# Performance work log

Hardware: AMD Instinct MI355X
Metric: run time of the kernel (lower is better)

Reference implementation:

```python
import jax, jax.numpy as jnp
import numpy as np

N = 262144  # collocation points
H = 128     # hidden width


def setup_inputs() -> dict:
    key = jax.random.key(0)
    ks = jax.random.split(key, 9)
    def glorot(k, shape):
        fan_in = shape[0]
        return jax.random.normal(k, shape, dtype=jnp.float32) / jnp.sqrt(jnp.float32(fan_in))
    return {
        "x": jax.random.normal(ks[0], (N, 3), dtype=jnp.float32),
        "W1": glorot(ks[1], (3, H)), "b1": jnp.zeros((H,), jnp.float32),
        "W2": glorot(ks[2], (H, H)), "b2": jnp.zeros((H,), jnp.float32),
        "W3": glorot(ks[3], (H, H)), "b3": jnp.zeros((H,), jnp.float32),
        "W4": glorot(ks[4], (H, 1)), "b4": jnp.zeros((1,), jnp.float32),
    }


def reference(x, W1, b1, W2, b2, W3, b3, W4, b4):
    def f(xi):  # xi: (3,) -> scalar c
        h = jnp.tanh(xi @ W1 + b1)
        h = jnp.tanh(h @ W2 + b2)
        h = jnp.tanh(h @ W3 + b3)
        return (h @ W4 + b4)[0]

    # forward value and full first-order gradient per point
    c, g = jax.vmap(jax.value_and_grad(f))(x)  # c: (N,), g: (N, 3)
    dc_dt, dc_dx, dc_dy = g[:, 0], g[:, 1], g[:, 2]

    # diagonal Hessian entries via forward-over-reverse HVPs
    e_x = jnp.array([0.0, 1.0, 0.0], dtype=x.dtype)
    e_y = jnp.array([0.0, 0.0, 1.0], dtype=x.dtype)

    def hvp(xi, v):
        return jax.jvp(jax.grad(f), (xi,), (v,))[1]

    d2c_dx2 = jax.vmap(lambda xi: hvp(xi, e_x)[1])(x)  # (N,)
    d2c_dy2 = jax.vmap(lambda xi: hvp(xi, e_y)[2])(x)  # (N,)

    return (c[:, None], dc_dt, dc_dx, dc_dy, d2c_dx2, d2c_dy2)
```

## Files before the change

### kernel.cpp

```cpp
#include <hip/hip_runtime.h>
#include <hip/hip_bf16.h>

#define TPB  256
#define WPB  4
#define NBLK 256
#define PROW 136
#define PSZ  (128 * PROW)

typedef short    short8 __attribute__((ext_vector_type(8)));
typedef float    f32x4  __attribute__((ext_vector_type(4)));
typedef unsigned uint4v __attribute__((ext_vector_type(4)));

#define SBAR() __builtin_amdgcn_sched_barrier(0)

struct Frag   { short8 k0, k1, k2, k3; };
struct Acc8   { f32x4 n0, n1, n2, n3, n4, n5, n6, n7; };
struct Acc8x6 { Acc8 a, b, c, d, e, f; };

__device__ __forceinline__ f32x4 sp4(float v) { f32x4 r = {v, v, v, v}; return r; }

__device__ __forceinline__ float fast_tanh(float z) {
    float e = __expf(2.0f * z);
    return 1.0f - 2.0f * __builtin_amdgcn_rcpf(e + 1.0f);
}
__device__ __forceinline__ f32x4 tanh4(f32x4 z) {
    f32x4 r;
    r[0] = fast_tanh(z[0]); r[1] = fast_tanh(z[1]);
    r[2] = fast_tanh(z[2]); r[3] = fast_tanh(z[3]);
    return r;
}

__device__ __forceinline__ unsigned short bf16_bits(float v) {
    __hip_bfloat16 b = __float2bfloat16(v);
    unsigned short s; __builtin_memcpy(&s, &b, 2);
    return s;
}
__device__ __forceinline__ unsigned pack_bf2(float lo, float hi) {
    return (unsigned)bf16_bits(lo) | ((unsigned)bf16_bits(hi) << 16);
}
__device__ __forceinline__ short8 packB(f32x4 lo, f32x4 hi) {
    uint4v u;
    u[0] = pack_bf2(lo[0], lo[1]);
    u[1] = pack_bf2(lo[2], lo[3]);
    u[2] = pack_bf2(hi[0], hi[1]);
    u[3] = pack_bf2(hi[2], hi[3]);
    return __builtin_bit_cast(short8, u);
}

__device__ __forceinline__ Acc8 acc_zero() {
    Acc8 A;
    A.n0 = sp4(0.f); A.n1 = sp4(0.f); A.n2 = sp4(0.f); A.n3 = sp4(0.f);
    A.n4 = sp4(0.f); A.n5 = sp4(0.f); A.n6 = sp4(0.f); A.n7 = sp4(0.f);
    return A;
}
__device__ __forceinline__ Acc8 acc_bias(const float* bp, int fb) {
    Acc8 A;
    A.n0 = *(const f32x4*)(bp + 0 * 16 + fb);
    A.n1 = *(const f32x4*)(bp + 1 * 16 + fb);
    A.n2 = *(const f32x4*)(bp + 2 * 16 + fb);
    A.n3 = *(const f32x4*)(bp + 3 * 16 + fb);
    A.n4 = *(const f32x4*)(bp + 4 * 16 + fb);
    A.n5 = *(const f32x4*)(bp + 5 * 16 + fb);
    A.n6 = *(const f32x4*)(bp + 6 * 16 + fb);
    A.n7 = *(const f32x4*)(bp + 7 * 16 + fb);
    return A;
}

__device__ __forceinline__ Acc8x6 gemm6_frag(const unsigned short* __restrict__ pnl,
                                             int c, int g,
                                             Frag B0, Frag B1, Frag B2,
                                             Frag B3, Frag B4, Frag B5,
                                             Acc8 A0, Acc8 A1, Acc8 A2,
                                             Acc8 A3, Acc8 A4, Acc8 A5) {
#define ROW6(NT, N, KK, V0, V1, V2, V3, V4, V5) { \
    const short8 af = *reinterpret_cast<const short8*>( \
        pnl + ((NT) * 16 + c) * PROW + (KK) * 32 + g * 8); \
    A0.N = __builtin_amdgcn_mfma_f32_16x16x32_bf16(af, V0, A0.N, 0, 0, 0); \
    A1.N = __builtin_amdgcn_mfma_f32_16x16x32_bf16(af, V1, A1.N, 0, 0, 0); \
    A2.N = __builtin_amdgcn_mfma_f32_16x16x32_bf16(af, V2, A2.N, 0, 0, 0); \
    A3.N = __builtin_amdgcn_mfma_f32_16x16x32_bf16(af, V3, A3.N, 0, 0, 0); \
    A4.N = __builtin_amdgcn_mfma_f32_16x16x32_bf16(af, V4, A4.N, 0, 0, 0); \
    A5.N = __builtin_amdgcn_mfma_f32_16x16x32_bf16(af, V5, A5.N, 0, 0, 0); }
#define KS6(KK, V0, V1, V2, V3, V4, V5) \
    ROW6(0, n0, KK, V0, V1, V2, V3, V4, V5) ROW6(1, n1, KK, V0, V1, V2, V3, V4, V5) \
    ROW6(2, n2, KK, V0, V1, V2, V3, V4, V5) ROW6(3, n3, KK, V0, V1, V2, V3, V4, V5) \
    ROW6(4, n4, KK, V0, V1, V2, V3, V4, V5) ROW6(5, n5, KK, V0, V1, V2, V3, V4, V5) \
    ROW6(6, n6, KK, V0, V1, V2, V3, V4, V5) ROW6(7, n7, KK, V0, V1, V2, V3, V4, V5) SBAR();
    KS6(0, B0.k0, B1.k0, B2.k0, B3.k0, B4.k0, B5.k0)
    KS6(1, B0.k1, B1.k1, B2.k1, B3.k1, B4.k1, B5.k1)
    KS6(2, B0.k2, B1.k2, B2.k2, B3.k2, B4.k2, B5.k2)
    KS6(3, B0.k3, B1.k3, B2.k3, B3.k3, B4.k3, B5.k3)
#undef KS6
#undef ROW6
    Acc8x6 R; R.a = A0; R.b = A1; R.c = A2; R.d = A3; R.e = A4; R.f = A5; return R;
}

__device__ __forceinline__ float red16(float v) {
    v += __shfl_xor(v, 16, 64);
    v += __shfl_xor(v, 32, 64);
    return v;
}
__device__ __forceinline__ float hsum4(f32x4 v) {
    return (v[0] + v[1]) + (v[2] + v[3]);
}

__global__ __launch_bounds__(TPB, 1) __attribute__((amdgpu_waves_per_eu(1)))
void mlp_jet_kernel(
    const float* __restrict__ X,
    const float* __restrict__ gW1, const float* __restrict__ gB1,
    const float* __restrict__ gW2, const float* __restrict__ gB2,
    const float* __restrict__ gW3, const float* __restrict__ gB3,
    const float* __restrict__ gW4, const float* __restrict__ gB4,
    float* __restrict__ out, int N)
{
    __shared__ alignas(16) unsigned short sPanel[2 * PSZ];
    __shared__ alignas(16) float sParam[7 * 128];

    const int tid = threadIdx.x;
    for (int idx = tid; idx < 2 * 128 * 128; idx += TPB) {
        int p = idx >> 14, e = idx & 16383, n = e >> 7, pp = e & 127;
        int kk = pp >> 5, gg = (pp >> 3) & 3, jj = pp & 7;
        int f = ((((jj >> 2) << 2) | kk) << 4) | (gg << 2) | (jj & 3);
        const float* Wsrc = p ? gW3 : gW2;
        sPanel[p * PSZ + n * PROW + pp] = bf16_bits(Wsrc[f * 128 + n]);
    }
    if (tid < 128) {
        sParam[0 * 128 + tid] = gW1[tid];
        sParam[1 * 128 + tid] = gW1[128 + tid];
        sParam[2 * 128 + tid] = gW1[256 + tid];
        sParam[3 * 128 + tid] = gB1[tid];
        sParam[4 * 128 + tid] = gB2[tid];
        sParam[5 * 128 + tid] = gB3[tid];
        sParam[6 * 128 + tid] = gW4[tid];
    }
    __syncthreads();

    const int lane = tid & 63;
    const int wave = tid >> 6;
    const int c = lane & 15, g = lane >> 4;
    const int fb = g << 2;
    const unsigned short* const pW2f = sPanel;
    const unsigned short* const pW3f = sPanel + PSZ;
    const float b4 = gB4[0];
    const float* const w4p = sParam + 6 * 128;

    const int tiles = N >> 4;
    for (int t = blockIdx.x * WPB + wave; t < tiles; t += NBLK * WPB) {
        const int sbase = t << 4;
        const float* xp = X + (long)(sbase + c) * 3;
        const float xt = xp[0], xx = xp[1], xy = xp[2];

        Frag h1F, t1t, t1x, t1y, s1x, s1y;
#define SEED(K, IL, IH) { \
    const int fL = (IL) * 16 + fb, fH = (IH) * 16 + fb; \
    f32x4 wtL = *(const f32x4*)(sParam + fL),        wtH = *(const f32x4*)(sParam + fH); \
    f32x4 wxL = *(const f32x4*)(sParam + 128 + fL),  wxH = *(const f32x4*)(sParam + 128 + fH); \
    f32x4 wyL = *(const f32x4*)(sParam + 256 + fL),  wyH = *(const f32x4*)(sParam + 256 + fH); \
    f32x4 bbL = *(const f32x4*)(sParam + 384 + fL),  bbH = *(const f32x4*)(sParam + 384 + fH); \
    f32x4 hL = tanh4(sp4(xt) * wtL + sp4(xx) * wxL + sp4(xy) * wyL + bbL); \
    f32x4 hH = tanh4(sp4(xt) * wtH + sp4(xx) * wxH + sp4(xy) * wyH + bbH); \
    f32x4 aL = sp4(1.f) - hL * hL, aH = sp4(1.f) - hH * hH; \
    h1F.K = packB(hL, hH); \
    t1t.K = packB(aL * wtL, aH * wtH); \
    t1x.K = packB(aL * wxL, aH * wxH); \
    t1y.K = packB(aL * wyL, aH * wyH); \
    s1x.K = packB((sp4(0.f) - hL) * aL * wxL * wxL, (sp4(0.f) - hH) * aH * wxH * wxH); \
    s1y.K = packB((sp4(0.f) - hL) * aL * wyL * wyL, (sp4(0.f) - hH) * aH * wyH * wyH); \
    SBAR(); }
        SEED(k0, 0, 4) SEED(k1, 1, 5) SEED(k2, 2, 6) SEED(k3, 3, 7)
#undef SEED

        Acc8x6 R6 = gemm6_frag(pW2f, c, g, h1F, t1t, t1x, t1y, s1x, s1y,
                               acc_bias(sParam + 4 * 128, fb),
                               acc_zero(), acc_zero(), acc_zero(),
                               acc_zero(), acc_zero());

        Frag h2F, t2t, txF, tyF, s2xF, s2yF;
#define POST2(K, NL, NH) { \
    f32x4 hL = tanh4(R6.a.NL), hH = tanh4(R6.a.NH); \
    f32x4 aL = sp4(1.f) - hL * hL, aH = sp4(1.f) - hH * hH; \
    h2F.K = packB(hL, hH); \
    t2t.K = packB(aL * R6.b.NL, aH * R6.b.NH); \
    f32x4 txL = aL * R6.c.NL, txH = aH * R6.c.NH; \
    txF.K = packB(txL, txH); \
    f32x4 pxL = (sp4(0.f) - hL) * txL * R6.c.NL, pxH = (sp4(0.f) - hH) * txH * R6.c.NH; \
    f32x4 tyL = aL * R6.d.NL, tyH = aH * R6.d.NH; \
    tyF.K = packB(tyL, tyH); \
    f32x4 pyL = (sp4(0.f) - hL) * tyL * R6.d.NL, pyH = (sp4(0.f) - hH) * tyH * R6.d.NH; \
    s2xF.K = packB(aL * R6.e.NL + pxL, aH * R6.e.NH + pxH); \
    s2yF.K = packB(aL * R6.f.NL + pyL, aH * R6.f.NH + pyH); \
    SBAR(); }
        POST2(k0, n0, n4) POST2(k1, n1, n5) POST2(k2, n2, n6) POST2(k3, n3, n7)
#undef POST2

        R6 = gemm6_frag(pW3f, c, g, h2F, t2t, txF, tyF, s2xF, s2yF,
                        acc_bias(sParam + 5 * 128, fb),
                        acc_zero(), acc_zero(), acc_zero(),
                        acc_zero(), acc_zero());

        {
            f32x4 scp = sp4(0.f), sc1t = sp4(0.f);
            f32x4 srxa = sp4(0.f), srxb = sp4(0.f);
            f32x4 srya = sp4(0.f), sryb = sp4(0.f);
            f32x4 sc2x = sp4(0.f), sc2y = sp4(0.f);
#define DOTS(NL, NH, IL, IH) { \
    f32x4 w4L = *(const f32x4*)(w4p + (IL) * 16 + fb); \
    f32x4 w4H = *(const f32x4*)(w4p + (IH) * 16 + fb); \
    f32x4 hL = tanh4(R6.a.NL), hH = tanh4(R6.a.NH); \
    f32x4 waL = w4L * (sp4(1.f) - hL * hL), waH = w4H * (sp4(1.f) - hH * hH); \
    scp  += w4L * hL + w4H * hH; \
    sc1t += waL * R6.b.NL + waH * R6.b.NH; \
    srxa += waL * R6.c.NL + waH * R6.c.NH; \
    srxb -= waL * hL * R6.c.NL * R6.c.NL + waH * hH * R6.c.NH * R6.c.NH; \
    srya += waL * R6.d.NL + waH * R6.d.NH; \
    sryb -= waL * hL * R6.d.NL * R6.d.NL + waH * hH * R6.d.NH * R6.d.NH; \
    sc2x += waL * R6.e.NL + waH * R6.e.NH; \
    sc2y += waL * R6.f.NL + waH * R6.f.NH; \
    SBAR(); }
            DOTS(n0, n4, 0, 4) DOTS(n1, n5, 1, 5) DOTS(n2, n6, 2, 6) DOTS(n3, n7, 3, 7)
#undef DOTS
            float cp  = red16(hsum4(scp));
            float c1t = red16(hsum4(sc1t));
            float c1x = red16(hsum4(srxa));
            float c1y = red16(hsum4(srya));
            float c2x = red16(hsum4(srxb) + hsum4(sc2x));
            float c2y = red16(hsum4(sryb) + hsum4(sc2y));
            if (lane < 16) {
                out[sbase + lane]           = cp + b4;
                out[(long)N + sbase + lane] = c1t;
                out[2L * N + sbase + lane]  = c1x;
                out[3L * N + sbase + lane]  = c1y;
                out[4L * N + sbase + lane]  = 2.f * c2x;
                out[5L * N + sbase + lane]  = 2.f * c2y;
            }
        }
    }
}

extern "C" void kernel_launch(void* const* d_in, const int* in_sizes, int n_in,
                              void* d_out, int out_size, void* d_ws, size_t ws_size,
                              hipStream_t stream) {
    const float* X  = (const float*)d_in[0];
    const float* W1 = (const float*)d_in[1];
    const float* B1 = (const float*)d_in[2];
    const float* W2 = (const float*)d_in[3];
    const float* B2 = (const float*)d_in[4];
    const float* W3 = (const float*)d_in[5];
    const float* B3 = (const float*)d_in[6];
    const float* W4 = (const float*)d_in[7];
    const float* B4 = (const float*)d_in[8];
    float* out = (float*)d_out;
    const int N = in_sizes[0] / 3;

    mlp_jet_kernel<<<NBLK, TPB, 0, stream>>>(X, W1, B1, W2, B2, W3, B3, W4, B4, out, N);
}
```

Measured before the change: 154.2 us.

## Prebuild bf16 weight panels in workspace and read MFMA A-fragments from global

A separate small kernel now converts W2/W3 to bf16 once per call and writes them into the workspace in a lane-contiguous fragment order. The main kernel drops its per-block LDS panel build and loads A-fragments straight from global memory (expected to be cache-resident), which frees about 70KB of LDS per block. The grid doubles to 512 blocks and waves_per_eu is relaxed to allow two waves. The risk is that global/L2 latency on every MFMA operand load may stall the MFMA chain that LDS reads used to feed, plus an extra kernel launch.

```diff
diff --git a/kernel.cpp b/kernel.cpp
--- a/kernel.cpp
+++ b/kernel.cpp
@@ -3,9 +3,7 @@
 
 #define TPB  256
 #define WPB  4
-#define NBLK 256
-#define PROW 136
-#define PSZ  (128 * PROW)
+#define NBLK 512
 
 typedef short    short8 __attribute__((ext_vector_type(8)));
 typedef float    f32x4  __attribute__((ext_vector_type(4)));
@@ -66,15 +64,34 @@
     return A;
 }
 
-__device__ __forceinline__ Acc8x6 gemm6_frag(const unsigned short* __restrict__ pnl,
-                                             int c, int g,
+__global__ void build_panels(const float* __restrict__ gW2,
+                             const float* __restrict__ gW3,
+                             unsigned short* __restrict__ ws) {
+    int idx = blockIdx.x * blockDim.x + threadIdx.x;
+    if (idx >= 2 * 16384) return;
+    int p = idx >> 14, e = idx & 16383;
+    int fidx = e >> 9;
+    int rem  = e & 511;
+    int lane = rem >> 3, j = rem & 7;
+    int NT = fidx >> 2, KK = fidx & 3;
+    int g = lane >> 4, c = lane & 15;
+    int n  = NT * 16 + c;
+    int pp = KK * 32 + g * 8 + j;
+    int kk = pp >> 5, gg = (pp >> 3) & 3, jj = pp & 7;
+    int f = ((((jj >> 2) << 2) | kk) << 4) | (gg << 2) | (jj & 3);
+    const float* Wsrc = p ? gW3 : gW2;
+    ws[idx] = bf16_bits(Wsrc[f * 128 + n]);
+}
+
+__device__ __forceinline__ Acc8x6 gemm6_frag(const unsigned short* __restrict__ gpnl,
+                                             int lane8,
                                              Frag B0, Frag B1, Frag B2,
                                              Frag B3, Frag B4, Frag B5,
                                              Acc8 A0, Acc8 A1, Acc8 A2,
                                              Acc8 A3, Acc8 A4, Acc8 A5) {
 #define ROW6(NT, N, KK, V0, V1, V2, V3, V4, V5) { \
     const short8 af = *reinterpret_cast<const short8*>( \
-        pnl + ((NT) * 16 + c) * PROW + (KK) * 32 + g * 8); \
+        gpnl + ((NT) * 4 + (KK)) * 512 + lane8); \
     A0.N = __builtin_amdgcn_mfma_f32_16x16x32_bf16(af, V0, A0.N, 0, 0, 0); \
     A1.N = __builtin_amdgcn_mfma_f32_16x16x32_bf16(af, V1, A1.N, 0, 0, 0); \
     A2.N = __builtin_amdgcn_mfma_f32_16x16x32_bf16(af, V2, A2.N, 0, 0, 0); \
@@ -104,26 +121,18 @@
     return (v[0] + v[1]) + (v[2] + v[3]);
 }
 
-__global__ __launch_bounds__(TPB, 1) __attribute__((amdgpu_waves_per_eu(1)))
+__global__ __launch_bounds__(TPB, 1) __attribute__((amdgpu_waves_per_eu(1, 2)))
 void mlp_jet_kernel(
     const float* __restrict__ X,
     const float* __restrict__ gW1, const float* __restrict__ gB1,
-    const float* __restrict__ gW2, const float* __restrict__ gB2,
-    const float* __restrict__ gW3, const float* __restrict__ gB3,
+    const float* __restrict__ gB2, const float* __restrict__ gB3,
     const float* __restrict__ gW4, const float* __restrict__ gB4,
+    const unsigned short* __restrict__ gPanel,
     float* __restrict__ out, int N)
 {
-    __shared__ alignas(16) unsigned short sPanel[2 * PSZ];
     __shared__ alignas(16) float sParam[7 * 128];
 
     const int tid = threadIdx.x;
-    for (int idx = tid; idx < 2 * 128 * 128; idx += TPB) {
-        int p = idx >> 14, e = idx & 16383, n = e >> 7, pp = e & 127;
-        int kk = pp >> 5, gg = (pp >> 3) & 3, jj = pp & 7;
-        int f = ((((jj >> 2) << 2) | kk) << 4) | (gg << 2) | (jj & 3);
-        const float* Wsrc = p ? gW3 : gW2;
-        sPanel[p * PSZ + n * PROW + pp] = bf16_bits(Wsrc[f * 128 + n]);
-    }
     if (tid < 128) {
         sParam[0 * 128 + tid] = gW1[tid];
         sParam[1 * 128 + tid] = gW1[128 + tid];
@@ -137,12 +146,14 @@
 
     const int lane = tid & 63;
     const int wave = tid >> 6;
-    const int c = lane & 15, g = lane >> 4;
+    const int g = lane >> 4;
     const int fb = g << 2;
-    const unsigned short* const pW2f = sPanel;
-    const unsigned short* const pW3f = sPanel + PSZ;
+    const int lane8 = lane * 8;
+    const unsigned short* const pW2f = gPanel;
+    const unsigned short* const pW3f = gPanel + 16384;
     const float b4 = gB4[0];
     const float* const w4p = sParam + 6 * 128;
+    const int c = lane & 15;
 
     const int tiles = N >> 4;
     for (int t = blockIdx.x * WPB + wave; t < tiles; t += NBLK * WPB) {
@@ -170,7 +181,7 @@
         SEED(k0, 0, 4) SEED(k1, 1, 5) SEED(k2, 2, 6) SEED(k3, 3, 7)
 #undef SEED
 
-        Acc8x6 R6 = gemm6_frag(pW2f, c, g, h1F, t1t, t1x, t1y, s1x, s1y,
+        Acc8x6 R6 = gemm6_frag(pW2f, lane8, h1F, t1t, t1x, t1y, s1x, s1y,
                                acc_bias(sParam + 4 * 128, fb),
                                acc_zero(), acc_zero(), acc_zero(),
                                acc_zero(), acc_zero());
@@ -193,7 +204,7 @@
         POST2(k0, n0, n4) POST2(k1, n1, n5) POST2(k2, n2, n6) POST2(k3, n3, n7)
 #undef POST2
 
-        R6 = gemm6_frag(pW3f, c, g, h2F, t2t, txF, tyF, s2xF, s2yF,
+        R6 = gemm6_frag(pW3f, lane8, h2F, t2t, txF, tyF, s2xF, s2yF,
                         acc_bias(sParam + 5 * 128, fb),
                         acc_zero(), acc_zero(), acc_zero(),
                         acc_zero(), acc_zero());
@@ -250,7 +261,9 @@
     const float* W4 = (const float*)d_in[7];
     const float* B4 = (const float*)d_in[8];
     float* out = (float*)d_out;
+    unsigned short* ws = (unsigned short*)d_ws;
     const int N = in_sizes[0] / 3;
 
-    mlp_jet_kernel<<<NBLK, TPB, 0, stream>>>(X, W1, B1, W2, B2, W3, B3, W4, B4, out, N);
-}
+    build_panels<<<(2 * 16384 + 255) / 256, 256, 0, stream>>>(W2, W3, ws);
+    mlp_jet_kernel<<<NBLK, TPB, 0, stream>>>(X, W1, B1, B2, B3, W4, B4, ws, out, N);
+}
```

New measurement: 350.8 us. 2.27x slower.
